# Optimization experiments

Measured on AMD Instinct MI355X. Metric: run time of the kernel, lower is better.

## Reference

```python
import jax, jax.numpy as jnp
import numpy as np

NUM_EXPERTS = 64
TOP_K = 2


def setup_inputs() -> dict:
    key = jax.random.key(0)
    k1, k2 = jax.random.split(key)
    hidden_states = jax.random.normal(k1, (4, 8192, 2048), dtype=jnp.float32)
    # torch nn.Linear weight layout: (num_experts, hidden)
    W = jax.random.normal(k2, (NUM_EXPERTS, 2048), dtype=jnp.float32) * 0.02
    return {"hidden_states": hidden_states, "W": W}


def reference(hidden_states, W):
    b, s, h = hidden_states.shape
    x = hidden_states.reshape(-1, h)                      # (T, H), T = b*s
    logits = jnp.einsum('th,eh->te', x, W)                # (T, E) skinny gate GEMM
    # eval mode: no gaussian noise added
    top_vals, indices = jax.lax.top_k(logits, TOP_K)      # (T, K)
    gates = jax.nn.softmax(top_vals, axis=-1)
    gates = gates.reshape(b, s, TOP_K)
    indices = indices.reshape(b, s, TOP_K)
    # load-balance auxiliary loss (faithful to source, incl. probs>0 mask)
    probs = jax.nn.softmax(logits, axis=-1)               # (T, E)
    mean_probs = probs.mean(axis=0)                       # (E,)
    routing_probs = (probs > 0).astype(logits.dtype).mean(axis=0)  # (E,)
    load_balance_loss = NUM_EXPERTS * jnp.sum(mean_probs * routing_probs)
    return (gates, indices, load_balance_loss)
```

## Files before the change

### kernel.cpp

```cpp
#include <hip/hip_runtime.h>
#include <math.h>

#define H       2048
#define E       64
#define NCHUNK  16
#define T_TOK   32768
#define GATES_OFF   0
#define IDX_OFF     65536
#define LOSS_OFF    131072

__global__ void zero_accum_kernel(float* __restrict__ accum) {
    accum[threadIdx.x] = 0.f;
}

__global__ __launch_bounds__(512, 4) void gate_main_kernel(
        const float* __restrict__ x,
        const float* __restrict__ W,
        float* __restrict__ out,
        float* __restrict__ accum)
{
    __shared__ float redf[4][64][64];

    const int tid   = threadIdx.x;
    const int lane  = tid & 63;
    const int wv    = tid >> 6;
    const int wvu   = __builtin_amdgcn_readfirstlane(wv);
    const int token = blockIdx.x * 64 + lane;

    const float4* xrow = (const float4*)(x + (size_t)token * H) + wvu * 4;
    const float4* Wv   = (const float4*)W;

    float acc[E];
#pragma unroll
    for (int e = 0; e < E; ++e) acc[e] = 0.f;

    for (int c = 0; c < NCHUNK; ++c) {
        const float4 xc0 = xrow[c * 32 + 0];
        const float4 xc1 = xrow[c * 32 + 1];
        const float4 xc2 = xrow[c * 32 + 2];
        const float4 xc3 = xrow[c * 32 + 3];

        const float4* wp = Wv + c * 32 + wvu * 4;
#pragma unroll
        for (int e = 0; e < E; ++e) {
            float4 w0 = wp[e * 512 + 0];
            float4 w1 = wp[e * 512 + 1];
            float4 w2 = wp[e * 512 + 2];
            float4 w3 = wp[e * 512 + 3];
            float a = acc[e];
            a = fmaf(xc0.x, w0.x, a);
            a = fmaf(xc0.y, w0.y, a);
            a = fmaf(xc0.z, w0.z, a);
            a = fmaf(xc0.w, w0.w, a);
            a = fmaf(xc1.x, w1.x, a);
            a = fmaf(xc1.y, w1.y, a);
            a = fmaf(xc1.z, w1.z, a);
            a = fmaf(xc1.w, w1.w, a);
            a = fmaf(xc2.x, w2.x, a);
            a = fmaf(xc2.y, w2.y, a);
            a = fmaf(xc2.z, w2.z, a);
            a = fmaf(xc2.w, w2.w, a);
            a = fmaf(xc3.x, w3.x, a);
            a = fmaf(xc3.y, w3.y, a);
            a = fmaf(xc3.z, w3.z, a);
            a = fmaf(xc3.w, w3.w, a);
            acc[e] = a;
        }
    }

    auto dump = [&](int b) {
#pragma unroll
        for (int e4 = 0; e4 < 16; ++e4) {
            int col = (e4 ^ (lane & 15)) * 4;
            *(float4*)&redf[b][lane][col] =
                make_float4(acc[e4*4], acc[e4*4+1], acc[e4*4+2], acc[e4*4+3]);
        }
    };
    auto gather = [&](int b) {
#pragma unroll
        for (int e4 = 0; e4 < 16; ++e4) {
            int col = (e4 ^ (lane & 15)) * 4;
            float4 v = *(const float4*)&redf[b][lane][col];
            acc[e4*4]   += v.x;
            acc[e4*4+1] += v.y;
            acc[e4*4+2] += v.z;
            acc[e4*4+3] += v.w;
        }
    };

    if (wv >= 4) dump(wv - 4);
    __syncthreads();
    if (wv < 4) gather(wv);
    __syncthreads();
    if (wv == 2 || wv == 3) dump(wv - 2);
    __syncthreads();
    if (wv < 2) gather(wv);
    __syncthreads();
    if (wv == 1) dump(0);
    __syncthreads();

    if (wv == 0) {
        gather(0);

        float v1 = acc[0]; int i1 = 0;
        float v2 = -INFINITY; int i2 = 0;
#pragma unroll
        for (int e = 1; e < E; ++e) {
            float v = acc[e];
            if (v > v1)      { v2 = v1; i2 = i1; v1 = v; i1 = e; }
            else if (v > v2) { v2 = v;  i2 = e; }
        }

        float s = 0.f;
#pragma unroll
        for (int e = 0; e < E; ++e) { acc[e] = __expf(acc[e] - v1); s += acc[e]; }
        float inv = 1.f / s;

#pragma unroll
        for (int e4 = 0; e4 < 16; ++e4) {
            int col = (e4 ^ (lane & 15)) * 4;
            float p0 = acc[e4*4]   * inv;
            float p1 = acc[e4*4+1] * inv;
            float p2 = acc[e4*4+2] * inv;
            float p3 = acc[e4*4+3] * inv;
            *(float4*)&redf[0][lane][col] = make_float4(p0, p1, p2, p3);
            *(float4*)&redf[1][lane][col] = make_float4(p0 > 0.f ? 1.f : 0.f,
                                                        p1 > 0.f ? 1.f : 0.f,
                                                        p2 > 0.f ? 1.f : 0.f,
                                                        p3 > 0.f ? 1.f : 0.f);
        }

        float t = __expf(v2 - v1);
        float d = 1.f / (1.f + t);
        *(float2*)&out[GATES_OFF + 2 * token] = make_float2(d, t * d);
        *(float2*)&out[IDX_OFF   + 2 * token] = make_float2((float)i1, (float)i2);
    }
    __syncthreads();

    {
        const int e = lane;
        float sp = 0.f, sc = 0.f;
#pragma unroll
        for (int t0 = 0; t0 < 8; ++t0) {
            int tt  = wv * 8 + t0;
            int idx = (((e >> 2) ^ (tt & 15)) << 2) + (e & 3);
            sp += redf[0][tt][idx];
            sc += redf[1][tt][idx];
        }
        atomicAdd(&accum[e],     sp);
        atomicAdd(&accum[E + e], sc);
    }
}

__global__ void gate_final_kernel(const float* __restrict__ accum, float* __restrict__ out) {
    int lane = threadIdx.x;
    const float invT = 1.f / (float)T_TOK;
    float mean_p  = accum[lane] * invT;
    float routing = accum[E + lane] * invT;
    float term = mean_p * routing;
#pragma unroll
    for (int d = 32; d > 0; d >>= 1) term += __shfl_xor(term, d, 64);
    if (lane == 0) out[LOSS_OFF] = 64.f * term;
}

extern "C" void kernel_launch(void* const* d_in, const int* in_sizes, int n_in,
                              void* d_out, int out_size, void* d_ws, size_t ws_size,
                              hipStream_t stream) {
    const float* x = (const float*)d_in[0];
    const float* W = (const float*)d_in[1];
    float* out   = (float*)d_out;
    float* accum = (float*)d_ws;

    zero_accum_kernel<<<1, 128, 0, stream>>>(accum);
    gate_main_kernel<<<T_TOK / 64, 512, 0, stream>>>(x, W, out, accum);
    gate_final_kernel<<<1, 64, 0, stream>>>(accum, out);
}
```

Measured before the change: 673.5 us.

## Stage token tiles in LDS asynchronously and split experts across waves

```diff
diff --git a/kernel.cpp b/kernel.cpp
--- a/kernel.cpp
+++ b/kernel.cpp
@@ -3,7 +3,7 @@
 
 #define H       2048
 #define E       64
-#define NCHUNK  16
+#define NCH     64
 #define T_TOK   32768
 #define GATES_OFF   0
 #define IDX_OFF     65536
@@ -13,123 +13,126 @@
     accum[threadIdx.x] = 0.f;
 }
 
+__device__ __forceinline__ void async_copy16(const float* g, void* l) {
+    __builtin_amdgcn_global_load_lds(
+        (const __attribute__((address_space(1))) unsigned int*)g,
+        (__attribute__((address_space(3))) unsigned int*)l,
+        16, 0, 0);
+}
+
 __global__ __launch_bounds__(512, 4) void gate_main_kernel(
         const float* __restrict__ x,
         const float* __restrict__ W,
         float* __restrict__ out,
         float* __restrict__ accum)
 {
-    __shared__ float redf[4][64][64];
+    __shared__ float xs[2][2048];
+    __shared__ float lg[64][68];
+    __shared__ float ct[64][68];
 
-    const int tid   = threadIdx.x;
-    const int lane  = tid & 63;
-    const int wv    = tid >> 6;
-    const int wvu   = __builtin_amdgcn_readfirstlane(wv);
-    const int token = blockIdx.x * 64 + lane;
+    const int tid  = threadIdx.x;
+    const int lane = tid & 63;
+    const int wv   = tid >> 6;
+    const int wvu  = __builtin_amdgcn_readfirstlane(wv);
+    const int tokBase = blockIdx.x * 64;
+    const float* xg = x + (size_t)tokBase * H;
 
-    const float4* xrow = (const float4*)(x + (size_t)token * H) + wvu * 4;
-    const float4* Wv   = (const float4*)W;
+    const int s_tok = tid >> 3;
+    const int s_q   = (tid & 7) ^ (s_tok & 7);
+    const float* s_src = xg + (size_t)s_tok * H + s_q * 4;
+    auto stage = [&](int c) {
+        async_copy16(s_src + c * 32, &xs[c & 1][tid * 4]);
+    };
 
-    float acc[E];
+    float acc[8];
 #pragma unroll
-    for (int e = 0; e < E; ++e) acc[e] = 0.f;
+    for (int e2 = 0; e2 < 8; ++e2) acc[e2] = 0.f;
 
-    for (int c = 0; c < NCHUNK; ++c) {
-        const float4 xc0 = xrow[c * 32 + 0];
-        const float4 xc1 = xrow[c * 32 + 1];
-        const float4 xc2 = xrow[c * 32 + 2];
-        const float4 xc3 = xrow[c * 32 + 3];
+    stage(0);
+    __syncthreads();
 
-        const float4* wp = Wv + c * 32 + wvu * 4;
+    const int   lsw   = lane & 7;
+    const float* xrow0 = &xs[0][lane * 32];
+    const float* wrow  = W + (size_t)(wvu * 8) * H;
+
+    for (int c = 0; c < NCH; ++c) {
+        if (c + 1 < NCH) stage(c + 1);
+
+        const float* xrow = xrow0 + (c & 1) * 2048;
+        float4 xq0 = *(const float4*)&xrow[((0 ^ lsw)) * 4];
+        float4 xq1 = *(const float4*)&xrow[((1 ^ lsw)) * 4];
+        float4 xq2 = *(const float4*)&xrow[((2 ^ lsw)) * 4];
+        float4 xq3 = *(const float4*)&xrow[((3 ^ lsw)) * 4];
+        float4 xq4 = *(const float4*)&xrow[((4 ^ lsw)) * 4];
+        float4 xq5 = *(const float4*)&xrow[((5 ^ lsw)) * 4];
+        float4 xq6 = *(const float4*)&xrow[((6 ^ lsw)) * 4];
+        float4 xq7 = *(const float4*)&xrow[((7 ^ lsw)) * 4];
+
 #pragma unroll
-        for (int e = 0; e < E; ++e) {
-            float4 w0 = wp[e * 512 + 0];
-            float4 w1 = wp[e * 512 + 1];
-            float4 w2 = wp[e * 512 + 2];
-            float4 w3 = wp[e * 512 + 3];
-            float a = acc[e];
-            a = fmaf(xc0.x, w0.x, a);
-            a = fmaf(xc0.y, w0.y, a);
-            a = fmaf(xc0.z, w0.z, a);
-            a = fmaf(xc0.w, w0.w, a);
-            a = fmaf(xc1.x, w1.x, a);
-            a = fmaf(xc1.y, w1.y, a);
-            a = fmaf(xc1.z, w1.z, a);
-            a = fmaf(xc1.w, w1.w, a);
-            a = fmaf(xc2.x, w2.x, a);
-            a = fmaf(xc2.y, w2.y, a);
-            a = fmaf(xc2.z, w2.z, a);
-            a = fmaf(xc2.w, w2.w, a);
-            a = fmaf(xc3.x, w3.x, a);
-            a = fmaf(xc3.y, w3.y, a);
-            a = fmaf(xc3.z, w3.z, a);
-            a = fmaf(xc3.w, w3.w, a);
-            acc[e] = a;
+        for (int e2 = 0; e2 < 8; ++e2) {
+            const float4* wp = (const float4*)(wrow + (size_t)e2 * H + c * 32);
+            float4 w0 = wp[0], w1 = wp[1], w2 = wp[2], w3 = wp[3];
+            float4 w4 = wp[4], w5 = wp[5], w6 = wp[6], w7 = wp[7];
+            float a = acc[e2];
+            a = fmaf(xq0.x, w0.x, a); a = fmaf(xq0.y, w0.y, a);
+            a = fmaf(xq0.z, w0.z, a); a = fmaf(xq0.w, w0.w, a);
+            a = fmaf(xq1.x, w1.x, a); a = fmaf(xq1.y, w1.y, a);
+            a = fmaf(xq1.z, w1.z, a); a = fmaf(xq1.w, w1.w, a);
+            a = fmaf(xq2.x, w2.x, a); a = fmaf(xq2.y, w2.y, a);
+            a = fmaf(xq2.z, w2.z, a); a = fmaf(xq2.w, w2.w, a);
+            a = fmaf(xq3.x, w3.x, a); a = fmaf(xq3.y, w3.y, a);
+            a = fmaf(xq3.z, w3.z, a); a = fmaf(xq3.w, w3.w, a);
+            a = fmaf(xq4.x, w4.x, a); a = fmaf(xq4.y, w4.y, a);
+            a = fmaf(xq4.z, w4.z, a); a = fmaf(xq4.w, w4.w, a);
+            a = fmaf(xq5.x, w5.x, a); a = fmaf(xq5.y, w5.y, a);
+            a = fmaf(xq5.z, w5.z, a); a = fmaf(xq5.w, w5.w, a);
+            a = fmaf(xq6.x, w6.x, a); a = fmaf(xq6.y, w6.y, a);
+            a = fmaf(xq6.z, w6.z, a); a = fmaf(xq6.w, w6.w, a);
+            a = fmaf(xq7.x, w7.x, a); a = fmaf(xq7.y, w7.y, a);
+            a = fmaf(xq7.z, w7.z, a); a = fmaf(xq7.w, w7.w, a);
+            acc[e2] = a;
         }
+        __syncthreads();
     }
 
-    auto dump = [&](int b) {
-#pragma unroll
-        for (int e4 = 0; e4 < 16; ++e4) {
-            int col = (e4 ^ (lane & 15)) * 4;
-            *(float4*)&redf[b][lane][col] =
-                make_float4(acc[e4*4], acc[e4*4+1], acc[e4*4+2], acc[e4*4+3]);
-        }
-    };
-    auto gather = [&](int b) {
-#pragma unroll
-        for (int e4 = 0; e4 < 16; ++e4) {
-            int col = (e4 ^ (lane & 15)) * 4;
-            float4 v = *(const float4*)&redf[b][lane][col];
-            acc[e4*4]   += v.x;
-            acc[e4*4+1] += v.y;
-            acc[e4*4+2] += v.z;
-            acc[e4*4+3] += v.w;
-        }
-    };
-
-    if (wv >= 4) dump(wv - 4);
-    __syncthreads();
-    if (wv < 4) gather(wv);
-    __syncthreads();
-    if (wv == 2 || wv == 3) dump(wv - 2);
-    __syncthreads();
-    if (wv < 2) gather(wv);
-    __syncthreads();
-    if (wv == 1) dump(0);
+    *(float4*)&lg[lane][wv * 8]     = make_float4(acc[0], acc[1], acc[2], acc[3]);
+    *(float4*)&lg[lane][wv * 8 + 4] = make_float4(acc[4], acc[5], acc[6], acc[7]);
     __syncthreads();
 
     if (wv == 0) {
-        gather(0);
+        float l[64];
+#pragma unroll
+        for (int i = 0; i < 16; ++i)
+            *(float4*)&l[i * 4] = *(const float4*)&lg[lane][i * 4];
 
-        float v1 = acc[0]; int i1 = 0;
+        float v1 = l[0]; int i1 = 0;
         float v2 = -INFINITY; int i2 = 0;
 #pragma unroll
         for (int e = 1; e < E; ++e) {
-            float v = acc[e];
+            float v = l[e];
             if (v > v1)      { v2 = v1; i2 = i1; v1 = v; i1 = e; }
             else if (v > v2) { v2 = v;  i2 = e; }
         }
 
         float s = 0.f;
 #pragma unroll
-        for (int e = 0; e < E; ++e) { acc[e] = __expf(acc[e] - v1); s += acc[e]; }
+        for (int e = 0; e < E; ++e) { l[e] = __expf(l[e] - v1); s += l[e]; }
         float inv = 1.f / s;
 
 #pragma unroll
-        for (int e4 = 0; e4 < 16; ++e4) {
-            int col = (e4 ^ (lane & 15)) * 4;
-            float p0 = acc[e4*4]   * inv;
-            float p1 = acc[e4*4+1] * inv;
-            float p2 = acc[e4*4+2] * inv;
-            float p3 = acc[e4*4+3] * inv;
-            *(float4*)&redf[0][lane][col] = make_float4(p0, p1, p2, p3);
-            *(float4*)&redf[1][lane][col] = make_float4(p0 > 0.f ? 1.f : 0.f,
-                                                        p1 > 0.f ? 1.f : 0.f,
-                                                        p2 > 0.f ? 1.f : 0.f,
-                                                        p3 > 0.f ? 1.f : 0.f);
+        for (int i = 0; i < 16; ++i) {
+            float p0 = l[i*4]   * inv;
+            float p1 = l[i*4+1] * inv;
+            float p2 = l[i*4+2] * inv;
+            float p3 = l[i*4+3] * inv;
+            *(float4*)&lg[lane][i * 4] = make_float4(p0, p1, p2, p3);
+            *(float4*)&ct[lane][i * 4] = make_float4(p0 > 0.f ? 1.f : 0.f,
+                                                     p1 > 0.f ? 1.f : 0.f,
+                                                     p2 > 0.f ? 1.f : 0.f,
+                                                     p3 > 0.f ? 1.f : 0.f);
         }
 
+        int token = tokBase + lane;
         float t = __expf(v2 - v1);
         float d = 1.f / (1.f + t);
         *(float2*)&out[GATES_OFF + 2 * token] = make_float2(d, t * d);
@@ -138,17 +141,15 @@
     __syncthreads();
 
     {
-        const int e = lane;
         float sp = 0.f, sc = 0.f;
 #pragma unroll
         for (int t0 = 0; t0 < 8; ++t0) {
-            int tt  = wv * 8 + t0;
-            int idx = (((e >> 2) ^ (tt & 15)) << 2) + (e & 3);
-            sp += redf[0][tt][idx];
-            sc += redf[1][tt][idx];
+            int t = wv * 8 + t0;
+            sp += lg[t][lane];
+            sc += ct[t][lane];
         }
-        atomicAdd(&accum[e],     sp);
-        atomicAdd(&accum[E + e], sc);
+        atomicAdd(&accum[lane],     sp);
+        atomicAdd(&accum[E + lane], sc);
     }
 }
 
```

Measured after the change: 756.1 us. +12.3%, slower.
